# Optimization experiments

Hardware: AMD Instinct MI355X
Metric: run time of the kernel (lower is better)

## Reference

```python
import jax, jax.numpy as jnp
import numpy as np

B, HN, N1, DIM = 4096, 16, 192, 256
EPS = 1e-5


def _xavier(key, fan_out, fan_in):
    limit = np.sqrt(6.0 / (fan_in + fan_out)).astype(np.float32)
    return jax.random.uniform(key, (fan_out, fan_in), jnp.float32, -limit, limit)


def setup_inputs() -> dict:
    key = jax.random.key(0)
    k_rgb, k_tir, k_idx, k_w1, k_w2 = jax.random.split(key, 5)
    attn_rgb_weight = jax.random.uniform(k_rgb, (B, HN, N1), jnp.float32)
    attn_tir_weight = jax.random.uniform(k_tir, (B, HN, N1), jnp.float32)
    # unique, sorted indices per batch into [0, DIM) (scatter with duplicate
    # indices is nondeterministic in torch, so we keep them unique)
    idx = jax.vmap(lambda k: jax.random.permutation(k, DIM)[:N1])(
        jax.random.split(k_idx, B))
    global_index_s = jnp.sort(idx, axis=-1).astype(jnp.int32)
    return {
        "attn_rgb_weight": attn_rgb_weight,
        "attn_tir_weight": attn_tir_weight,
        "global_index_s": global_index_s,
        "ln_g": jnp.ones((2 * DIM,), jnp.float32),
        "ln_b": jnp.zeros((2 * DIM,), jnp.float32),
        "W1": _xavier(k_w1, DIM, 2 * DIM),   # Linear(512 -> 256), torch (out,in)
        "b1": jnp.zeros((DIM,), jnp.float32),
        "W2": _xavier(k_w2, 2 * DIM, DIM),   # Linear(256 -> 512)
        "b2": jnp.zeros((2 * DIM,), jnp.float32),
    }


def reference(attn_rgb_weight, attn_tir_weight, global_index_s,
              ln_g, ln_b, W1, b1, W2, b2):
    b, hn, n1 = attn_rgb_weight.shape
    idx = global_index_s[:, None, :]                     # [B, 1, N1]
    bi = jnp.arange(b)[:, None, None]                    # [B, 1, 1]
    hi = jnp.arange(hn)[None, :, None]                   # [1, hn, 1]
    # scatter sparse attention weights into dense [B, hn, DIM] buffers
    vex_rgb = jnp.zeros((b, hn, DIM), attn_rgb_weight.dtype)
    vex_rgb = vex_rgb.at[bi, hi, idx].set(attn_rgb_weight)
    vex_tir = jnp.zeros((b, hn, DIM), attn_tir_weight.dtype)
    vex_tir = vex_tir.at[bi, hi, idx].set(attn_tir_weight)
    vex = jnp.concatenate([vex_rgb, vex_tir], axis=-1)   # [B, hn, 2*DIM]
    # LayerNorm(2*DIM) -> Linear -> ReLU -> Linear -> Sigmoid
    mu = jnp.mean(vex, axis=-1, keepdims=True)
    var = jnp.mean(jnp.square(vex - mu), axis=-1, keepdims=True)
    x = (vex - mu) * jax.lax.rsqrt(var + EPS) * ln_g + ln_b
    h = jax.nn.relu(jnp.einsum('bhe,de->bhd', x, W1) + b1)
    o = jax.nn.sigmoid(jnp.einsum('bhd,ed->bhe', h, W2) + b2)  # [B, hn, 2*DIM]
    # gather back via index
    idx_full = jnp.broadcast_to(idx, (b, hn, n1))
    out_rgb = jnp.take_along_axis(o[:, :, :DIM], idx_full, axis=-1)
    out_tir = jnp.take_along_axis(o[:, :, DIM:], idx_full, axis=-1)
    return (out_rgb, out_tir)
```

## Files before the change

### kernel.cpp

```cpp
#include <hip/hip_runtime.h>
#include <stdint.h>

#define NJ 192
#define OUT_HALF 12582912

#define XS 520
#define OSD 516

#define H_BYTE 32768
#define STAT_OFF 67072
#define ARENA  67584

typedef __attribute__((ext_vector_type(4)))  float    f32x4;
typedef __attribute__((ext_vector_type(16))) float    f32x16;
typedef __attribute__((ext_vector_type(2)))  float    f32x2;
typedef __attribute__((ext_vector_type(4)))  int      i32x4;
typedef __attribute__((ext_vector_type(4)))  uint32_t u32x4;
typedef __attribute__((ext_vector_type(8)))  short    bf16x8;

__device__ float g_u1[256];
__device__ float g_v1[256];

__device__ __forceinline__ uint32_t cvt_pk_bf16(float lo, float hi) {
    uint32_t r;
    asm("v_cvt_pk_bf16_f32 %0, %1, %2" : "=v"(r) : "v"(lo), "v"(hi));
    return r;
}
__device__ __forceinline__ void gload16(const void* g, void* l) {
    __builtin_amdgcn_global_load_lds(
        (const __attribute__((address_space(1))) uint32_t*)g,
        (__attribute__((address_space(3))) uint32_t*)l, 16, 0, 0);
}

__global__ __launch_bounds__(256)
void pack_weights(const float* __restrict__ W1, const float* __restrict__ W2,
                  const float* __restrict__ ln_g, const float* __restrict__ ln_b,
                  const float* __restrict__ b1, short* __restrict__ ws) {
    if (blockIdx.x == 128) {
        int d = threadIdx.x;
        float u = b1[d], v = 0.f;
        const float* wr = W1 + d * 512;
        for (int e = 0; e < 512; e += 4) {
            f32x4 w4 = *(const f32x4*)(wr + e);
            f32x4 g4 = *(const f32x4*)(ln_g + e);
            f32x4 l4 = *(const f32x4*)(ln_b + e);
            #pragma unroll
            for (int t = 0; t < 4; ++t) { v += w4[t] * g4[t]; u += w4[t] * l4[t]; }
        }
        g_u1[d] = u; g_v1[d] = v;
        return;
    }
    int id = blockIdx.x * 256 + threadIdx.x;
    if (id < 16384) {
        int u8 = id >> 9, w = id & 511;
        int c = u8 >> 1, h = u8 & 1;
        int t2 = w >> 6, lane = w & 63;
        int nt = 2 * t2 + h;
        int row = nt * 16 + (lane & 15);
        int k0 = c * 16 + ((lane >> 4) << 2);
        f32x4 a  = *(const f32x4*)(W1 + row * 512 + k0);
        f32x4 b  = *(const f32x4*)(W1 + row * 512 + 256 + k0);
        f32x4 ga = *(const f32x4*)(ln_g + k0);
        f32x4 gb = *(const f32x4*)(ln_g + 256 + k0);
        u32x4 o;
        #pragma unroll
        for (int t = 0; t < 4; ++t) o[t] = cvt_pk_bf16(a[t] * ga[t], b[t] * gb[t]);
        *(u32x4*)(ws + id * 8) = o;
    } else {
        int id2 = id - 16384;
        int u = id2 >> 9;
        int g = id2 & 511;
        int f = g >> 6, lane = g & 63;
        int k = u >> 1, h = u & 1;
        int t = h * 8 + f;
        int n = t * 32 + (lane & 31);
        int orow = (n >> 1) + (n & 1) * 256;
        int k0 = k * 16 + ((lane >> 5) << 3);
        f32x4 a = *(const f32x4*)(W2 + orow * 256 + k0);
        f32x4 b = *(const f32x4*)(W2 + orow * 256 + k0 + 4);
        u32x4 o;
        o[0] = cvt_pk_bf16(a[0], a[1]);
        o[1] = cvt_pk_bf16(a[2], a[3]);
        o[2] = cvt_pk_bf16(b[0], b[1]);
        o[3] = cvt_pk_bf16(b[2], b[3]);
        *(u32x4*)(ws + 131072 + id2 * 8) = o;
    }
}

__global__ __launch_bounds__(512, 4)
void fused_mlp(const float* __restrict__ rgb,
               const float* __restrict__ tir,
               const int*  __restrict__ gidx,
               const short* __restrict__ P1,
               const short* __restrict__ P2,
               const float* __restrict__ b2,
               float* __restrict__ out)
{
    __shared__ __attribute__((aligned(16))) char arena[ARENA];
    short* sX    = (short*)arena;
    short* sHsh  = (short*)(arena + H_BYTE);
    float* sStat = (float*)(arena + STAT_OFF);
    float* sO    = (float*)arena;

    const int tid  = threadIdx.x;
    const int blk  = blockIdx.x;
    const int row0 = blk * 64;
    const int b0   = blk * 4;
    const int wave = tid >> 6;
    const int lane = tid & 63;
    const int lr   = lane & 15;
    const int quad = lane >> 4;
    const int mw   = wave & 3;
    const int nw   = wave >> 2;
    const int mh   = wave >> 2;
    const int nq   = wave & 3;

    const char* P1b = (const char*)P1;
    const char* P2b = (const char*)P2;

    {
        uint32_t* xd = (uint32_t*)sX;
        #pragma unroll
        for (int i = 0; i < 8; ++i) {
            int u = i * 512 + tid;
            int r = u >> 6, g = u & 63;
            *(u32x4*)(xd + r * 260 + g * 4) = (u32x4){0u, 0u, 0u, 0u};
        }
    }
    __syncthreads();

    {
        int r = tid >> 3, sub = tid & 7;
        int j0 = sub * 24;
        uint32_t* xdw = (uint32_t*)(sX + r * XS);
        const int*   gp = gidx + (b0 + (r >> 4)) * NJ + j0;
        const float* rp = rgb + (row0 + r) * NJ + j0;
        const float* tp = tir + (row0 + r) * NJ + j0;
        float s = 0.f, ss = 0.f;
        #pragma unroll
        for (int q = 0; q < 6; ++q) {
            i32x4 iv = *(const i32x4*)(gp + q * 4);
            f32x4 vr = *(const f32x4*)(rp + q * 4);
            f32x4 vt = *(const f32x4*)(tp + q * 4);
            #pragma unroll
            for (int e = 0; e < 4; ++e) {
                s  += vr[e] + vt[e];
                ss += vr[e] * vr[e] + vt[e] * vt[e];
                xdw[iv[e]] = cvt_pk_bf16(vr[e], vt[e]);
            }
        }
        s  += __shfl_xor(s, 1, 8);  ss += __shfl_xor(ss, 1, 8);
        s  += __shfl_xor(s, 2, 8);  ss += __shfl_xor(ss, 2, 8);
        s  += __shfl_xor(s, 4, 8);  ss += __shfl_xor(ss, 4, 8);
        float mu  = s * (1.f / 512.f);
        float var = ss * (1.f / 512.f) - mu * mu;
        float rs  = rsqrtf(var + 1e-5f);
        if (sub == 0) { sStat[2 * r] = rs; sStat[2 * r + 1] = mu * rs; }
    }
    __syncthreads();

    bf16x8 a1[16];
    {
        const short* xr = sX + (mw * 16 + lr) * XS + quad * 8;
        #pragma unroll
        for (int c = 0; c < 16; ++c) a1[c] = *(const bf16x8*)(xr + c * 32);
    }
    __syncthreads();

    gload16(P1b + 0 * 8192 + tid * 16, arena + 0 * 8192 + wave * 1024);
    gload16(P1b + 1 * 8192 + tid * 16, arena + 1 * 8192 + wave * 1024);
    gload16(P1b + 2 * 8192 + tid * 16, arena + 2 * 8192 + wave * 1024);

    f32x4 acc1[8];
    #pragma unroll
    for (int i = 0; i < 8; ++i) acc1[i] = (f32x4){0.f, 0.f, 0.f, 0.f};

    #pragma unroll
    for (int j = 0; j < 32; ++j) {
        const int c = j >> 1, h = j & 1;
        asm volatile("s_waitcnt vmcnt(2)" ::: "memory");
        __builtin_amdgcn_s_barrier();
        if (j <= 28) {
            gload16(P1b + (j + 3) * 8192 + tid * 16,
                    arena + ((j + 3) & 3) * 8192 + wave * 1024);
        } else {
            gload16(P2b + (j - 29) * 8192 + tid * 16,
                    arena + ((j + 3) & 3) * 8192 + wave * 1024);
        }
        const short* sb = (const short*)arena + ((j & 3) << 12);
        bf16x8 w0 = *(const bf16x8*)(sb + (nw * 4 + 0) * 512 + lane * 8);
        bf16x8 w1 = *(const bf16x8*)(sb + (nw * 4 + 1) * 512 + lane * 8);
        bf16x8 w2 = *(const bf16x8*)(sb + (nw * 4 + 2) * 512 + lane * 8);
        bf16x8 w3 = *(const bf16x8*)(sb + (nw * 4 + 3) * 512 + lane * 8);
        asm volatile("s_waitcnt lgkmcnt(0)" ::: "memory");
        __builtin_amdgcn_sched_barrier(0);
        acc1[0 + h] = __builtin_amdgcn_mfma_f32_16x16x32_bf16(a1[c], w0, acc1[0 + h], 0, 0, 0);
        acc1[2 + h] = __builtin_amdgcn_mfma_f32_16x16x32_bf16(a1[c], w1, acc1[2 + h], 0, 0, 0);
        acc1[4 + h] = __builtin_amdgcn_mfma_f32_16x16x32_bf16(a1[c], w2, acc1[4 + h], 0, 0, 0);
        acc1[6 + h] = __builtin_amdgcn_mfma_f32_16x16x32_bf16(a1[c], w3, acc1[6 + h], 0, 0, 0);
    }

    {
        const int baserow = mw * 16 + quad * 4;
        float rsv[4], mrs[4];
        #pragma unroll
        for (int rr = 0; rr < 4; ++rr) {
            rsv[rr] = sStat[2 * (baserow + rr)];
            mrs[rr] = sStat[2 * (baserow + rr) + 1];
        }
        #pragma unroll
        for (int i = 0; i < 8; ++i) {
            int col = (nw * 8 + i) * 16 + lr;
            int blkc = col >> 3, within = col & 7;
            float u1c = g_u1[col], v1c = g_v1[col];
            #pragma unroll
            for (int rr = 0; rr < 4; ++rr) {
                int r = baserow + rr;
                float hh = rsv[rr] * acc1[i][rr] + (u1c - mrs[rr] * v1c);
                hh = fmaxf(hh, 0.f);
                sHsh[r * 256 + ((blkc ^ (r & 31)) << 3) + within] = (short)cvt_pk_bf16(hh, hh);
            }
        }
    }
    __syncthreads();

    f32x16 acc2[4];
    #pragma unroll
    for (int i = 0; i < 4; ++i)
        #pragma unroll
        for (int e = 0; e < 16; ++e) acc2[i][e] = 0.f;

    bf16x8 a2frag;
    #pragma unroll
    for (int u = 0; u < 32; ++u) {
        const int k = u >> 1, h = u & 1;
        if (u <= 29)      asm volatile("s_waitcnt vmcnt(2)" ::: "memory");
        else if (u == 30) asm volatile("s_waitcnt vmcnt(1)" ::: "memory");
        else              asm volatile("s_waitcnt vmcnt(0)" ::: "memory");
        __builtin_amdgcn_s_barrier();
        if (u <= 28) {
            gload16(P2b + (u + 3) * 8192 + tid * 16,
                    arena + ((u + 3) & 3) * 8192 + wave * 1024);
        }
        if (h == 0) {
            int r = mh * 32 + (lane & 31);
            int blkc = (k * 2 + (lane >> 5)) ^ (r & 31);
            a2frag = *(const bf16x8*)(sHsh + r * 256 + blkc * 8);
        }
        const short* sb = (const short*)arena + ((u & 3) << 12);
        bf16x8 bf0 = *(const bf16x8*)(sb + (nq * 2 + 0) * 512 + lane * 8);
        bf16x8 bf1 = *(const bf16x8*)(sb + (nq * 2 + 1) * 512 + lane * 8);
        asm volatile("s_waitcnt lgkmcnt(0)" ::: "memory");
        __builtin_amdgcn_sched_barrier(0);
        acc2[h * 2 + 0] = __builtin_amdgcn_mfma_f32_32x32x16_bf16(a2frag, bf0, acc2[h * 2 + 0], 0, 0, 0);
        acc2[h * 2 + 1] = __builtin_amdgcn_mfma_f32_32x32x16_bf16(a2frag, bf1, acc2[h * 2 + 1], 0, 0, 0);
    }
    __syncthreads();

    #pragma unroll
    for (int p = 0; p < 2; ++p) {
        if (mh == p) {
            #pragma unroll
            for (int ai = 0; ai < 4; ++ai) {
                int t = (ai >> 1) * 8 + nq * 2 + (ai & 1);
                int colp = t * 32 + (lane & 31);
                float b2v = b2[(colp >> 1) + (colp & 1) * 256];
                #pragma unroll
                for (int rg = 0; rg < 16; ++rg) {
                    int lrow = (rg & 3) + 8 * (rg >> 2) + 4 * (lane >> 5);
                    float x = acc2[ai][rg] + b2v;
                    sO[lrow * OSD + colp] = 1.f / (1.f + __expf(-x));
                }
            }
        }
        __syncthreads();
        #pragma unroll
        for (int it = 0; it < 3; ++it) {
            int q4 = (it * 512 + tid) * 4;
            int rl = q4 / NJ;
            int jj = q4 - rl * NJ;
            int r  = p * 32 + rl;
            i32x4 iv = *(const i32x4*)(gidx + (b0 + (r >> 4)) * NJ + jj);
            const float* orow = sO + rl * OSD;
            f32x4 vr, vt;
            #pragma unroll
            for (int e = 0; e < 4; ++e) {
                f32x2 pr = *(const f32x2*)(orow + 2 * iv[e]);
                vr[e] = pr[0]; vt[e] = pr[1];
            }
            *(f32x4*)&out[(row0 + r) * NJ + jj]            = vr;
            *(f32x4*)&out[OUT_HALF + (row0 + r) * NJ + jj] = vt;
        }
        if (p == 0) __syncthreads();
    }
}

extern "C" void kernel_launch(void* const* d_in, const int* in_sizes, int n_in,
                              void* d_out, int out_size, void* d_ws, size_t ws_size,
                              hipStream_t stream) {
    const float* rgb  = (const float*)d_in[0];
    const float* tir  = (const float*)d_in[1];
    const int*   gidx = (const int*)d_in[2];
    const float* ln_g = (const float*)d_in[3];
    const float* ln_b = (const float*)d_in[4];
    const float* W1   = (const float*)d_in[5];
    const float* b1   = (const float*)d_in[6];
    const float* W2   = (const float*)d_in[7];
    const float* b2   = (const float*)d_in[8];
    float* out = (float*)d_out;
    short* wsp = (short*)d_ws;

    pack_weights<<<129, 256, 0, stream>>>(W1, W2, ln_g, ln_b, b1, wsp);
    fused_mlp<<<1024, 512, 0, stream>>>(rgb, tir, gidx,
                                        wsp, wsp + 131072, b2, out);
}
```

Measured before the change: 257.5 us.

## Load packed weights directly from global into registers instead of LDS pipeline

Both MFMA GEMM loops drop the 4-stage global_load_lds ring buffer with per-step barriers. Each wave now reads its weight fragments straight from global memory (L2-cached) into registers, and the A fragments come straight from LDS. This removes 64 block-wide barriers and the LDS staging traffic. In exchange the kernel depends on L2/global latency being hidden by the compiler's scheduling, and every wave redundantly fetches weights.

```diff
diff --git a/kernel.cpp b/kernel.cpp
--- a/kernel.cpp
+++ b/kernel.cpp
@@ -25,11 +25,6 @@
     uint32_t r;
     asm("v_cvt_pk_bf16_f32 %0, %1, %2" : "=v"(r) : "v"(lo), "v"(hi));
     return r;
-}
-__device__ __forceinline__ void gload16(const void* g, void* l) {
-    __builtin_amdgcn_global_load_lds(
-        (const __attribute__((address_space(1))) uint32_t*)g,
-        (__attribute__((address_space(3))) uint32_t*)l, 16, 0, 0);
 }
 
 __global__ __launch_bounds__(256)
@@ -115,9 +110,6 @@
     const int mh   = wave >> 2;
     const int nq   = wave & 3;
 
-    const char* P1b = (const char*)P1;
-    const char* P2b = (const char*)P2;
-
     {
         uint32_t* xd = (uint32_t*)sX;
         #pragma unroll
@@ -159,46 +151,26 @@
     }
     __syncthreads();
 
-    bf16x8 a1[16];
-    {
-        const short* xr = sX + (mw * 16 + lr) * XS + quad * 8;
-        #pragma unroll
-        for (int c = 0; c < 16; ++c) a1[c] = *(const bf16x8*)(xr + c * 32);
-    }
-    __syncthreads();
-
-    gload16(P1b + 0 * 8192 + tid * 16, arena + 0 * 8192 + wave * 1024);
-    gload16(P1b + 1 * 8192 + tid * 16, arena + 1 * 8192 + wave * 1024);
-    gload16(P1b + 2 * 8192 + tid * 16, arena + 2 * 8192 + wave * 1024);
-
     f32x4 acc1[8];
     #pragma unroll
     for (int i = 0; i < 8; ++i) acc1[i] = (f32x4){0.f, 0.f, 0.f, 0.f};
 
-    #pragma unroll
-    for (int j = 0; j < 32; ++j) {
-        const int c = j >> 1, h = j & 1;
-        asm volatile("s_waitcnt vmcnt(2)" ::: "memory");
-        __builtin_amdgcn_s_barrier();
-        if (j <= 28) {
-            gload16(P1b + (j + 3) * 8192 + tid * 16,
-                    arena + ((j + 3) & 3) * 8192 + wave * 1024);
-        } else {
-            gload16(P2b + (j - 29) * 8192 + tid * 16,
-                    arena + ((j + 3) & 3) * 8192 + wave * 1024);
-        }
-        const short* sb = (const short*)arena + ((j & 3) << 12);
-        bf16x8 w0 = *(const bf16x8*)(sb + (nw * 4 + 0) * 512 + lane * 8);
-        bf16x8 w1 = *(const bf16x8*)(sb + (nw * 4 + 1) * 512 + lane * 8);
-        bf16x8 w2 = *(const bf16x8*)(sb + (nw * 4 + 2) * 512 + lane * 8);
-        bf16x8 w3 = *(const bf16x8*)(sb + (nw * 4 + 3) * 512 + lane * 8);
-        asm volatile("s_waitcnt lgkmcnt(0)" ::: "memory");
-        __builtin_amdgcn_sched_barrier(0);
-        acc1[0 + h] = __builtin_amdgcn_mfma_f32_16x16x32_bf16(a1[c], w0, acc1[0 + h], 0, 0, 0);
-        acc1[2 + h] = __builtin_amdgcn_mfma_f32_16x16x32_bf16(a1[c], w1, acc1[2 + h], 0, 0, 0);
-        acc1[4 + h] = __builtin_amdgcn_mfma_f32_16x16x32_bf16(a1[c], w2, acc1[4 + h], 0, 0, 0);
-        acc1[6 + h] = __builtin_amdgcn_mfma_f32_16x16x32_bf16(a1[c], w3, acc1[6 + h], 0, 0, 0);
-    }
+    {
+        const short* xrow = sX + (mw * 16 + lr) * XS + quad * 8;
+        const short* p1l  = P1 + ((nw * 4) << 9) + lane * 8;
+        #pragma unroll
+        for (int c = 0; c < 16; ++c) {
+            bf16x8 a = *(const bf16x8*)(xrow + c * 32);
+            bf16x8 wf[8];
+            #pragma unroll
+            for (int i = 0; i < 8; ++i)
+                wf[i] = *(const bf16x8*)(p1l + ((2 * c + (i & 1)) << 12) + ((i >> 1) << 9));
+            #pragma unroll
+            for (int i = 0; i < 8; ++i)
+                acc1[i] = __builtin_amdgcn_mfma_f32_16x16x32_bf16(a, wf[i], acc1[i], 0, 0, 0);
+        }
+    }
+    __syncthreads();
 
     {
         const int baserow = mw * 16 + quad * 4;
@@ -230,30 +202,24 @@
         #pragma unroll
         for (int e = 0; e < 16; ++e) acc2[i][e] = 0.f;
 
-    bf16x8 a2frag;
-    #pragma unroll
-    for (int u = 0; u < 32; ++u) {
-        const int k = u >> 1, h = u & 1;
-        if (u <= 29)      asm volatile("s_waitcnt vmcnt(2)" ::: "memory");
-        else if (u == 30) asm volatile("s_waitcnt vmcnt(1)" ::: "memory");
-        else              asm volatile("s_waitcnt vmcnt(0)" ::: "memory");
-        __builtin_amdgcn_s_barrier();
-        if (u <= 28) {
-            gload16(P2b + (u + 3) * 8192 + tid * 16,
-                    arena + ((u + 3) & 3) * 8192 + wave * 1024);
-        }
-        if (h == 0) {
-            int r = mh * 32 + (lane & 31);
+    {
+        const int r = mh * 32 + (lane & 31);
+        const short* hrow = sHsh + r * 256;
+        const short* p2l  = P2 + lane * 8;
+        #pragma unroll
+        for (int k = 0; k < 16; ++k) {
             int blkc = (k * 2 + (lane >> 5)) ^ (r & 31);
-            a2frag = *(const bf16x8*)(sHsh + r * 256 + blkc * 8);
-        }
-        const short* sb = (const short*)arena + ((u & 3) << 12);
-        bf16x8 bf0 = *(const bf16x8*)(sb + (nq * 2 + 0) * 512 + lane * 8);
-        bf16x8 bf1 = *(const bf16x8*)(sb + (nq * 2 + 1) * 512 + lane * 8);
-        asm volatile("s_waitcnt lgkmcnt(0)" ::: "memory");
-        __builtin_amdgcn_sched_barrier(0);
-        acc2[h * 2 + 0] = __builtin_amdgcn_mfma_f32_32x32x16_bf16(a2frag, bf0, acc2[h * 2 + 0], 0, 0, 0);
-        acc2[h * 2 + 1] = __builtin_amdgcn_mfma_f32_32x32x16_bf16(a2frag, bf1, acc2[h * 2 + 1], 0, 0, 0);
+            bf16x8 a2 = *(const bf16x8*)(hrow + blkc * 8);
+            bf16x8 wf[4];
+            #pragma unroll
+            for (int j = 0; j < 4; ++j) {
+                int t = (j >> 1) * 8 + nq * 2 + (j & 1);
+                wf[j] = *(const bf16x8*)(p2l + ((2 * k + (t >> 3)) << 12) + ((t & 7) << 9));
+            }
+            #pragma unroll
+            for (int j = 0; j < 4; ++j)
+                acc2[j] = __builtin_amdgcn_mfma_f32_32x32x16_bf16(a2, wf[j], acc2[j], 0, 0, 0);
+        }
     }
     __syncthreads();
 
```

Measured after the change: 273.2 us. 1.06x slower.
